# Kernel tuning notes

Hardware: AMD Instinct MI355X
Metric: run time of the kernel (lower is better)

Reference implementation:

```python
import jax, jax.numpy as jnp
import numpy as np
from jax import lax

DN = ('NCHW', 'OIHW', 'NCHW')


def conv_s2(x, w, b):
    # Conv2d(kernel=4, stride=2, padding=1): halves H,W
    y = lax.conv_general_dilated(x, w, (2, 2), ((1, 1), (1, 1)), dimension_numbers=DN)
    return y + b[None, :, None, None]


def conv_1x1(x, w, b):
    y = lax.conv_general_dilated(x, w, (1, 1), ((0, 0), (0, 0)), dimension_numbers=DN)
    return y + b[None, :, None, None]


def convT_s2(x, w, b):
    # torch ConvTranspose2d(kernel=4, stride=2, padding=1); torch weight layout [I,O,kh,kw]
    wt = jnp.flip(w, (2, 3)).transpose(1, 0, 2, 3)  # -> [O,I,kh,kw], spatially flipped
    y = lax.conv_general_dilated(x, wt, (1, 1), ((2, 2), (2, 2)),
                                 lhs_dilation=(2, 2), dimension_numbers=DN)
    return y + b[None, :, None, None]


def setup_inputs() -> dict:
    key = jax.random.key(0)
    ks = jax.random.split(key, 20)
    f32 = jnp.float32
    s = 0.05  # small init scale to keep activations sane
    inp = {
        'x': jax.random.uniform(ks[0], (32, 3, 256, 256), dtype=f32),
        # encoder
        'ew1': jax.random.normal(ks[1], (128, 3, 4, 4), f32) * s,
        'eb1': jnp.zeros((128,), f32),
        'ew2': jax.random.normal(ks[2], (256, 128, 4, 4), f32) * s,
        'eb2': jnp.zeros((256,), f32),
        'ew3': jax.random.normal(ks[3], (512, 256, 4, 4), f32) * s,
        'eb3': jnp.zeros((512,), f32),
        # pre-VQ 1x1 conv
        'pw': jax.random.normal(ks[4], (64, 512, 1, 1), f32) * s,
        'pb': jnp.zeros((64,), f32),
        # codebook (torch.randn in module)
        'emb': jax.random.normal(ks[5], (512, 64), f32),
        # decoder (ConvTranspose2d weights: [in, out, kh, kw])
        'dw1': jax.random.normal(ks[6], (64, 256, 4, 4), f32) * s,
        'db1': jnp.zeros((256,), f32),
        'dw2': jax.random.normal(ks[7], (256, 128, 4, 4), f32) * s,
        'db2': jnp.zeros((128,), f32),
        'dw3': jax.random.normal(ks[8], (128, 3, 4, 4), f32) * s,
        'db3': jnp.zeros((3,), f32),
    }
    return inp


def reference(x, ew1, eb1, ew2, eb2, ew3, eb3, pw, pb, emb,
              dw1, db1, dw2, db2, dw3, db3):
    # encoder
    h = jax.nn.relu(conv_s2(x, ew1, eb1))
    h = jax.nn.relu(conv_s2(h, ew2, eb2))
    h = jax.nn.relu(conv_s2(h, ew3, eb3))
    z_e = conv_1x1(h, pw, pb)  # [B, D, H, W]

    b, d, hh, ww = z_e.shape
    x_flat = z_e.reshape(b, d, hh * ww).transpose(0, 2, 1)  # [B, HW, D]
    # squared distances via expansion (same math, no [B,HW,K,D] blowup)
    x2 = jnp.sum(x_flat ** 2, axis=-1, keepdims=True)        # [B, HW, 1]
    e2 = jnp.sum(emb ** 2, axis=-1)                          # [K]
    dist = x2 - 2.0 * jnp.einsum('bnd,kd->bnk', x_flat, emb) + e2[None, None, :]
    indices = jnp.argmin(dist, axis=2)                       # [B, HW]
    zq_flat = emb[indices]                                   # [B, HW, D]
    z_q = zq_flat.transpose(0, 2, 1).reshape(b, d, hh, ww)

    quant_loss = (jnp.mean((zq_flat - x_flat) ** 2) * 2.0)   # matches detach-symmetric mse in fwd value

    # decoder
    y = jax.nn.relu(convT_s2(z_q, dw1, db1))
    y = jax.nn.relu(convT_s2(y, dw2, db2))
    y = jax.nn.sigmoid(convT_s2(y, dw3, db3))
    return (y, quant_loss)
```

## Files before the change

### kernel.cpp

```cpp
#include <hip/hip_runtime.h>
#include <cstddef>
#include <cstdint>

typedef __attribute__((ext_vector_type(8))) _Float16 half8;
typedef __attribute__((ext_vector_type(4))) float f32x4;

static __device__ __forceinline__ unsigned packhl(float v) {
  _Float16 h = (_Float16)v;
  _Float16 l = (_Float16)((v - (float)h) * 2048.0f);
  return (unsigned)__builtin_bit_cast(unsigned short, h) |
         ((unsigned)__builtin_bit_cast(unsigned short, l) << 16);
}


template<int CIN>
__global__ __launch_bounds__(256) void wsplit_k(
    const float* __restrict__ W, _Float16* __restrict__ Wh,
    _Float16* __restrict__ Wl, int Cout) {
  constexpr int NCB = CIN / 32;
  int idx = blockIdx.x * 256 + threadIdx.x;
  if (idx >= Cout * CIN) return;
  int ci = idx % CIN, co = idx / CIN;
  int cb = ci >> 5, k8 = (ci >> 3) & 3, j = ci & 7;
  const float* wp = W + (size_t)idx * 16;
#pragma unroll
  for (int tap = 0; tap < 16; ++tap) {
    float w = wp[tap];
    _Float16 wh = (_Float16)w;
    _Float16 wl = (_Float16)((w - (float)wh) * 2048.0f);
    size_t o = (((size_t)(tap * NCB + cb) * 4 + k8) * Cout + co) * 8 + j;
    Wh[o] = wh; Wl[o] = wl;
  }
}

template<int CIN>
__global__ __launch_bounds__(256) void wsplitT_k(
    const float* __restrict__ W, _Float16* __restrict__ Wh,
    _Float16* __restrict__ Wl, int Cout) {
  constexpr int NCB = CIN / 32;
  int idx = blockIdx.x * 256 + threadIdx.x;
  if (idx >= CIN * Cout) return;
  int co = idx % Cout, ci = idx / Cout;
  int cb = ci >> 5, k8 = (ci >> 3) & 3, j = ci & 7;
  const float* wp = W + (size_t)idx * 16;
#pragma unroll
  for (int t = 0; t < 16; ++t) {
    int py = (t >> 3) & 1, px = (t >> 2) & 1, i0 = (t >> 1) & 1, i1 = t & 1;
    int kh = py ? (i0 ? 2 : 0) : (i0 ? 3 : 1);
    int kw = px ? (i1 ? 2 : 0) : (i1 ? 3 : 1);
    float w = wp[kh * 4 + kw];
    _Float16 wh = (_Float16)w;
    _Float16 wl = (_Float16)((w - (float)wh) * 2048.0f);
    size_t o = (((size_t)(t * NCB + cb) * 4 + k8) * Cout + co) * 8 + j;
    Wh[o] = wh; Wl[o] = wl;
  }
}

__global__ __launch_bounds__(256) void border_k(
    char* base, int c8n, int H2, int W2, size_t SAI, size_t LOFF, int nimg) {
  int nb = 2 * W2 + 2 * (H2 - 2);
  int tot = nimg * c8n * 2 * nb;
  int idx = blockIdx.x * 256 + threadIdx.x;
  if (idx >= tot) return;
  int s = idx % nb; int r = idx / nb;
  int pl = r & 1; r >>= 1;
  int c8 = r % c8n; int b = r / c8n;
  int y, x;
  if (s < W2)            { y = 0;       x = s; }
  else if (s < 2 * W2)   { y = H2 - 1;  x = s - W2; }
  else { int t = s - 2 * W2; y = 1 + (t >> 1); x = (t & 1) ? W2 - 1 : 0; }
  size_t PLANE = (size_t)H2 * W2 * 16;
  char* p = base + (size_t)b * SAI + (size_t)pl * LOFF + (size_t)c8 * PLANE
            + ((size_t)y * W2 + x) * 16;
  *(uint4*)p = make_uint4(0, 0, 0, 0);
}

template<int CIN, int COUT, int CGRP, int NF, int RELU, int PACKOUT, int SPLITIN,
         int XMAP>
__global__ __launch_bounds__(256) void conv_mfma2(
    const void* __restrict__ inP, const _Float16* __restrict__ Whg,
    const _Float16* __restrict__ Wlg, const float* __restrict__ bias,
    float* __restrict__ out, int Hin, int Win, size_t inSAI, size_t inLOFF) {
  constexpr int NCB  = CIN / 32;
  constexpr int MT   = COUT / CGRP;
  constexpr int MF   = MT / 64;
  constexpr int ROWS = 2 * NF + 2;
  constexpr int NPOS = ROWS * 34;
  constexpr int K8S  = NPOS + 6;
  const int Hout = Hin >> 1, Wout = Win >> 1;
  const int TW = Wout >> 4;
  __shared__ half8 Bh[4 * K8S], Bl[4 * K8S];
  const int tid = threadIdx.x;
  const int lane = tid & 63, w = tid >> 6;
  const int l15 = lane & 15, k8 = lane >> 4;
  int tx, ty, cg, b;
  {
    unsigned nwg = gridDim.x * gridDim.y;
    unsigned id  = blockIdx.y * gridDim.x + blockIdx.x;
    unsigned sw  = (id & 7) * (nwg >> 3) + (id >> 3);
    const int bx = sw % gridDim.x, by = sw / gridDim.x;
    tx = bx % TW; ty = bx / TW;
    cg = by % CGRP;
    b  = by / CGRP;
  }
  const int oy0 = ty * NF, ox0 = tx << 4;
  const int iy_org = 2 * oy0 - 1, ix_org = 2 * ox0 - 1;
  const int cbase = cg * MT + w * (MT / 4);
  const size_t HW = (size_t)Hin * Win;
  const size_t tapStride = (size_t)NCB * 4 * COUT * 8;

  unsigned goff[4];
  const char* baseh = nullptr;
  size_t PLANE = 0;
  if (SPLITIN) {
    const int W2 = Win + 2;
    PLANE = (size_t)(Hin + 2) * W2 * 16;
    constexpr int S0[4] = {0, 64, 128, NPOS - 64};
#pragma unroll
    for (int t = 0; t < 4; ++t) {
      int s = S0[t] + lane;
      int r = s / 17, c = s - r * 17;
      int hy = r >> 1, p = r & 1;
      int hx = (c << 1) | p;
      int iy = iy_org + hy + 1, ix = ix_org + hx + 1;
      goff[t] = (unsigned)(((size_t)iy * W2 + ix) * 16);
    }
    baseh = (const char*)inP + ((size_t)b * inSAI) + (size_t)w * PLANE;
  }

  f32x4 accM[MF][NF], accX[MF][NF];
#pragma unroll
  for (int m = 0; m < MF; ++m)
#pragma unroll
    for (int nf = 0; nf < NF; ++nf) {
      accM[m][nf] = f32x4{0,0,0,0};
      accX[m][nf] = f32x4{0,0,0,0};
    }

  for (int cb = 0; cb < NCB; ++cb) {
    __syncthreads();
    if (SPLITIN) {
      const char* pc = baseh + (size_t)cb * 4 * PLANE;
      char* lh = (char*)&Bh[w * K8S];
      char* ll = (char*)&Bl[w * K8S];
      constexpr int S0[4] = {0, 64, 128, NPOS - 64};
#pragma unroll
      for (int t = 0; t < 4; ++t) {
        __builtin_amdgcn_global_load_lds(
            (const __attribute__((address_space(1))) void*)(pc + goff[t]),
            (__attribute__((address_space(3))) void*)(lh + S0[t] * 16), 16, 0, 0);
        __builtin_amdgcn_global_load_lds(
            (const __attribute__((address_space(1))) void*)(pc + inLOFF + goff[t]),
            (__attribute__((address_space(3))) void*)(ll + S0[t] * 16), 16, 0, 0);
      }
    } else {
      const unsigned* inU = (const unsigned*)inP;
      for (int u = tid; u < NPOS * 4; u += 256) {
        int kk = u / NPOS, pos = u - kk * NPOS;
        int hy = pos / 34, hx = pos - hy * 34;
        int iy = iy_org + hy, ix = ix_org + hx;
        bool ok = (unsigned)iy < (unsigned)Hin && (unsigned)ix < (unsigned)Win;
        uint4 qa = {0,0,0,0}, qb = {0,0,0,0};
        if (ok) {
          const uint4* gp = (const uint4*)(inU +
              (((size_t)b * (CIN / 8) + cb * 4 + kk) * HW + (size_t)iy * Win + ix) * 8);
          qa = gp[0]; qb = gp[1];
        }
        unsigned av[8] = {qa.x, qa.y, qa.z, qa.w, qb.x, qb.y, qb.z, qb.w};
        half8 vh, vl;
#pragma unroll
        for (int j = 0; j < 8; ++j) {
          vh[j] = __builtin_bit_cast(_Float16, (unsigned short)(av[j] & 0xffffu));
          vl[j] = __builtin_bit_cast(_Float16, (unsigned short)(av[j] >> 16));
        }
        int slotBase = (hy * 2 + (hx & 1)) * 17 + (hx >> 1);
        Bh[kk * K8S + slotBase] = vh;
        Bl[kk * K8S + slotBase] = vl;
      }
    }
    __syncthreads();
    const _Float16* aph = Whg + (((size_t)cb * 4 + k8) * COUT + cbase + l15) * 8;
    const _Float16* apl = Wlg + (((size_t)cb * 4 + k8) * COUT + cbase + l15) * 8;
    half8 ah[2][MF], al[2][MF];
#pragma unroll
    for (int m = 0; m < MF; ++m) {
      ah[0][m] = *(const half8*)(aph + m * 128);
      al[0][m] = *(const half8*)(apl + m * 128);
    }
#pragma unroll
    for (int tp = 0; tp < 16; ++tp) {
      const int cur = tp & 1, nxt = cur ^ 1;
      if (tp < 15) {
#pragma unroll
        for (int m = 0; m < MF; ++m) {
          ah[nxt][m] = *(const half8*)(aph + (size_t)(tp + 1) * tapStride + m * 128);
          al[nxt][m] = *(const half8*)(apl + (size_t)(tp + 1) * tapStride + m * 128);
        }
      }
      const int kh = tp >> 2, kw = tp & 3;
      const int p = kw & 1, cidx = kw >> 1;
#pragma unroll
      for (int nf = 0; nf < NF; ++nf) {
        const int slot = k8 * K8S + ((2 * nf + kh) * 2 + p) * 17 + l15 + cidx;
        const half8 bh = Bh[slot], bl = Bl[slot];
#pragma unroll
        for (int m = 0; m < MF; ++m) {
          accM[m][nf] = __builtin_amdgcn_mfma_f32_16x16x32_f16(ah[cur][m], bh, accM[m][nf], 0, 0, 0);
          accX[m][nf] = __builtin_amdgcn_mfma_f32_16x16x32_f16(ah[cur][m], bl, accX[m][nf], 0, 0, 0);
          accX[m][nf] = __builtin_amdgcn_mfma_f32_16x16x32_f16(al[cur][m], bh, accX[m][nf], 0, 0, 0);
        }
      }
    }
  }
#pragma unroll
  for (int m = 0; m < MF; ++m)
#pragma unroll
    for (int nf = 0; nf < NF; ++nf) {
      int oy = oy0 + nf, ox = ox0 + l15;
      if (PACKOUT) {
        unsigned pk[4];
#pragma unroll
        for (int i = 0; i < 4; ++i) {
          int co = cbase + m * 16 + k8 * 4 + i;
          float v = accM[m][nf][i] + accX[m][nf][i] * (1.0f / 2048.0f) + bias[co];
          if (RELU) v = fmaxf(v, 0.0f);
          pk[i] = packhl(v);
        }
        int co8 = (cbase + m * 16 + k8 * 4) >> 3;
        int j0 = (k8 & 1) * 4;
        unsigned* outU = (unsigned*)out;
        *(uint4*)(outU + (((size_t)b * (COUT / 8) + co8) * ((size_t)Hout * Wout)
                          + (size_t)oy * Wout + ox) * 8 + j0) =
            make_uint4(pk[0], pk[1], pk[2], pk[3]);
      } else {
#pragma unroll
        for (int i = 0; i < 4; ++i) {
          int co = cbase + m * 16 + k8 * 4 + i;
          float v = accM[m][nf][i] + accX[m][nf][i] * (1.0f / 2048.0f) + bias[co];
          if (RELU) v = fmaxf(v, 0.0f);
          out[(((size_t)b * COUT + co) * Hout + oy) * Wout + ox] = v;
        }
      }
    }
}

template<int CIN, int COUT, int CGRP, int RELU, int PACKIN, int PACKOUT, int SWZ>
__global__ __launch_bounds__(256) void convT_mfma(
    const float* __restrict__ in, const _Float16* __restrict__ Whg,
    const _Float16* __restrict__ Wlg, const float* __restrict__ bias,
    float* __restrict__ out, int Hin, int Win) {
  constexpr int NCB = CIN / 32;
  constexpr int MT  = COUT / CGRP;
  constexpr int MF  = MT / 64;
  const int Hout = Hin * 2, Wout = Win * 2;
  const int TW = Win >> 4;
  __shared__ half8 Bh[4 * 72], Bl[4 * 72];
  const int tid = threadIdx.x;
  const int lane = tid & 63, w = tid >> 6;
  const int l15 = lane & 15, k8 = lane >> 4;
  int bx = blockIdx.x, by = blockIdx.y;
  if (SWZ) {
    unsigned nwg = gridDim.x * gridDim.y;
    unsigned id  = (unsigned)by * gridDim.x + bx;
    unsigned sw  = (id & 7) * (nwg >> 3) + (id >> 3);
    bx = (int)(sw % gridDim.x); by = (int)(sw / gridDim.x);
  }
  const int tx = bx % TW, ty = bx / TW;
  const int cg = by % CGRP;
  const int b  = by / CGRP;
  const int ty0 = ty << 1, tx0 = tx << 4;
  const int cbase = cg * MT + w * (MT / 4);
  const size_t HW = (size_t)Hin * Win;
  const size_t tapStride = (size_t)NCB * 4 * COUT * 8;

  f32x4 accM[MF][4][2], accX[MF][4][2];
#pragma unroll
  for (int m = 0; m < MF; ++m)
#pragma unroll
    for (int p = 0; p < 4; ++p)
#pragma unroll
      for (int nf = 0; nf < 2; ++nf) {
        accM[m][p][nf] = f32x4{0,0,0,0};
        accX[m][p][nf] = f32x4{0,0,0,0};
      }

  for (int cb = 0; cb < NCB; ++cb) {
    __syncthreads();
    for (int u = tid; u < 288; u += 256) {
      int pos = u % 72, kk = u / 72;
      int r = pos / 18, c = pos - r * 18;
      int iy = ty0 - 1 + r, ix = tx0 - 1 + c;
      bool ok = (unsigned)iy < (unsigned)Hin && (unsigned)ix < (unsigned)Win;
      half8 vh, vl;
      if (PACKIN) {
        uint4 qa = {0,0,0,0}, qb = {0,0,0,0};
        if (ok) {
          const uint4* gp = (const uint4*)((const unsigned*)in +
              (((size_t)b * (CIN / 8) + cb * 4 + kk) * HW + (size_t)iy * Win + ix) * 8);
          qa = gp[0]; qb = gp[1];
        }
        unsigned av[8] = {qa.x, qa.y, qa.z, qa.w, qb.x, qb.y, qb.z, qb.w};
#pragma unroll
        for (int j = 0; j < 8; ++j) {
          vh[j] = __builtin_bit_cast(_Float16, (unsigned short)(av[j] & 0xffffu));
          vl[j] = __builtin_bit_cast(_Float16, (unsigned short)(av[j] >> 16));
        }
      } else {
        const float* gp = in + ((size_t)b * CIN + cb * 32 + kk * 8) * HW
                          + (ptrdiff_t)iy * Win + ix;
#pragma unroll
        for (int j = 0; j < 8; ++j) {
          float x = ok ? gp[(size_t)j * HW] : 0.0f;
          _Float16 xh = (_Float16)x;
          vh[j] = xh; vl[j] = (_Float16)((x - (float)xh) * 2048.0f);
        }
      }
      Bh[kk * 72 + pos] = vh;
      Bl[kk * 72 + pos] = vl;
    }
    __syncthreads();
    const _Float16* aph = Whg + (((size_t)cb * 4 + k8) * COUT + cbase + l15) * 8;
    const _Float16* apl = Wlg + (((size_t)cb * 4 + k8) * COUT + cbase + l15) * 8;
    half8 ah[2][MF], al[2][MF];
#pragma unroll
    for (int m = 0; m < MF; ++m) {
      ah[0][m] = *(const half8*)(aph + m * 128);
      al[0][m] = *(const half8*)(apl + m * 128);
    }
#pragma unroll
    for (int t = 0; t < 16; ++t) {
      const int cur = t & 1, nxt = cur ^ 1;
      if (t < 15) {
#pragma unroll
        for (int m = 0; m < MF; ++m) {
          ah[nxt][m] = *(const half8*)(aph + (size_t)(t + 1) * tapStride + m * 128);
          al[nxt][m] = *(const half8*)(apl + (size_t)(t + 1) * tapStride + m * 128);
        }
      }
      const int py = (t >> 3) & 1, px = (t >> 2) & 1;
      const int i0 = (t >> 1) & 1, i1 = t & 1;
      const int dy = py ? (i0 ? 0 : 1) : (i0 ? -1 : 0);
      const int dx = px ? (i1 ? 0 : 1) : (i1 ? -1 : 0);
      const int p = py * 2 + px;
#pragma unroll
      for (int nf = 0; nf < 2; ++nf) {
        int slot = k8 * 72 + (nf + 1 + dy) * 18 + (l15 + 1 + dx);
        half8 bh = Bh[slot], bl = Bl[slot];
#pragma unroll
        for (int m = 0; m < MF; ++m) {
          accM[m][p][nf] = __builtin_amdgcn_mfma_f32_16x16x32_f16(ah[cur][m], bh, accM[m][p][nf], 0, 0, 0);
          accX[m][p][nf] = __builtin_amdgcn_mfma_f32_16x16x32_f16(ah[cur][m], bl, accX[m][p][nf], 0, 0, 0);
          accX[m][p][nf] = __builtin_amdgcn_mfma_f32_16x16x32_f16(al[cur][m], bh, accX[m][p][nf], 0, 0, 0);
        }
      }
    }
  }
#pragma unroll
  for (int m = 0; m < MF; ++m) {
    const int co0m = cbase + m * 16;
#pragma unroll
    for (int nf = 0; nf < 2; ++nf) {
#pragma unroll
      for (int i = 0; i < 4; ++i) {
        int co = co0m + k8 * 4 + i;
        float bb = bias[co];
#pragma unroll
        for (int py = 0; py < 2; ++py) {
          float v0 = accM[m][py * 2 + 0][nf][i] + accX[m][py * 2 + 0][nf][i] * (1.0f / 2048.0f) + bb;
          float v1 = accM[m][py * 2 + 1][nf][i] + accX[m][py * 2 + 1][nf][i] * (1.0f / 2048.0f) + bb;
          if (RELU) { v0 = fmaxf(v0, 0.0f); v1 = fmaxf(v1, 0.0f); }
          int oy = 2 * (ty0 + nf) + py, ox = 2 * (tx0 + l15);
          if (PACKOUT) {
            unsigned* outU = (unsigned*)out;
            int co8 = (co0m >> 3) + (k8 >> 1);
            int j = (k8 * 4 + i) & 7;
            size_t base = ((size_t)b * (COUT / 8) + co8) * ((size_t)Hout * Wout);
            outU[(base + (size_t)oy * Wout + ox) * 8 + j]     = packhl(v0);
            outU[(base + (size_t)oy * Wout + ox + 1) * 8 + j] = packhl(v1);
          } else {
            *(float2*)(out + (((size_t)b * COUT + co) * Hout + oy) * Wout + ox) =
                make_float2(v0, v1);
          }
        }
      }
    }
  }
}


template<int CIN, int G, int RELU, int PACKOUT>
__global__ __launch_bounds__(256) void conv_t(
    const float* __restrict__ in, const float* __restrict__ wt,
    const float* __restrict__ bias, float* __restrict__ out,
    int Cout, int Hin, int Win, size_t oSAI, size_t oLOFF) {
  const int Hout = Hin >> 1, Wout = Win >> 1;
  const int TW = Wout >> 4;
  __shared__ float tile[34 * 35];
  int tid = threadIdx.x;
  int oxl = tid & 15, oyl = tid >> 4;
  int tyt = blockIdx.x / TW, txt = blockIdx.x - tyt * TW;
  int oy0 = tyt << 4, ox0 = txt << 4;
  int cg = blockIdx.y % (Cout / G);
  int b  = blockIdx.y / (Cout / G);
  int co0 = cg * G;
  const int iy_org = 2 * oy0 - 1, ix_org = 2 * ox0 - 1;
  const float* ip = in + (size_t)b * CIN * Hin * Win;
  float acc[G];
#pragma unroll
  for (int j = 0; j < G; ++j) acc[j] = bias[co0 + j];
  const int lbase = (2 * oyl) * 35 + 2 * oxl;
  for (int ci = 0; ci < CIN; ++ci) {
    const float* ic = ip + (size_t)ci * Hin * Win;
    __syncthreads();
#pragma unroll
    for (int k = 0; k < 5; ++k) {
      int idx = tid + k * 256;
      if (idx < 34 * 34) {
        int r = idx / 34, c = idx - r * 34;
        int iy = iy_org + r, ix = ix_org + c;
        float v = ((unsigned)iy < (unsigned)Hin && (unsigned)ix < (unsigned)Win)
                      ? ic[(size_t)iy * Win + ix] : 0.0f;
        tile[r * 35 + c] = v;
      }
    }
    __syncthreads();
    float xv[16];
#pragma unroll
    for (int kh = 0; kh < 4; ++kh)
#pragma unroll
      for (int kw = 0; kw < 4; ++kw)
        xv[kh * 4 + kw] = tile[lbase + kh * 35 + kw];
    const float* wc = wt + ((size_t)co0 * CIN + ci) * 16;
#pragma unroll
    for (int j = 0; j < G; ++j) {
      const float* wj = wc + (size_t)j * CIN * 16;
#pragma unroll
      for (int t2 = 0; t2 < 16; ++t2) acc[j] = fmaf(xv[t2], wj[t2], acc[j]);
    }
  }
  int oy = oy0 + oyl, ox = ox0 + oxl;
  if (RELU) {
#pragma unroll
    for (int j = 0; j < G; ++j) acc[j] = fmaxf(acc[j], 0.0f);
  }
  if (PACKOUT == 2) {
    const int W2 = Wout + 2;
    const size_t PLANE = (size_t)(Hout + 2) * W2 * 16;
    char* ob0 = (char*)out + (size_t)b * oSAI
                + ((size_t)(oy + 1) * W2 + ox + 1) * 16;
#pragma unroll
    for (int mb = 0; mb < G / 8; ++mb) {
      half8 hv, lv;
#pragma unroll
      for (int j = 0; j < 8; ++j) {
        float v = acc[mb * 8 + j];
        _Float16 h = (_Float16)v;
        hv[j] = h; lv[j] = (_Float16)((v - (float)h) * 2048.0f);
      }
      char* ob = ob0 + (size_t)((co0 >> 3) + mb) * PLANE;
      *(half8*)ob = hv;
      *(half8*)(ob + oLOFF) = lv;
    }
  } else {
    size_t cs = (size_t)Hout * Wout;
    float* op = out + ((size_t)(b * Cout + co0) * Hout + oy) * Wout + ox;
#pragma unroll
    for (int j = 0; j < G; ++j) op[(size_t)j * cs] = acc[j];
  }
}

template<int CIN, int G>
__global__ __launch_bounds__(256) void conv1x1_k(
    const float* __restrict__ in, const float* __restrict__ wt,
    const float* __restrict__ bias, float* __restrict__ out,
    int Cout, int HW) {
  int hw = blockIdx.x * 256 + threadIdx.x;
  int cg = blockIdx.y % (Cout / G);
  int b  = blockIdx.y / (Cout / G);
  int co0 = cg * G;
  const float* ip = in + (size_t)b * CIN * HW + hw;
  float acc[G];
#pragma unroll
  for (int j = 0; j < G; ++j) acc[j] = bias[co0 + j];
#pragma unroll 4
  for (int ci = 0; ci < CIN; ++ci) {
    float xv = ip[(size_t)ci * HW];
#pragma unroll
    for (int j = 0; j < G; ++j)
      acc[j] = fmaf(xv, wt[(size_t)(co0 + j) * CIN + ci], acc[j]);
  }
  float* op = out + ((size_t)(b * Cout + co0)) * HW + hw;
#pragma unroll
  for (int j = 0; j < G; ++j) op[(size_t)j * HW] = acc[j];
}

__global__ __launch_bounds__(128) void vq_k(
    const float* __restrict__ ze, const float* __restrict__ emb,
    float* __restrict__ zq, float* __restrict__ partial) {
  __shared__ float4 se4[128 * 16];
  __shared__ float red[128];
  int tid = threadIdx.x;
  int gid = blockIdx.x * 128 + tid;
  int b = gid >> 10, n = gid & 1023;
  const float* zp = ze + ((size_t)b << 16) + n;
  float4 v4[16];
#pragma unroll
  for (int d = 0; d < 16; ++d) {
    v4[d].x = zp[(size_t)(4 * d + 0) << 10];
    v4[d].y = zp[(size_t)(4 * d + 1) << 10];
    v4[d].z = zp[(size_t)(4 * d + 2) << 10];
    v4[d].w = zp[(size_t)(4 * d + 3) << 10];
  }
  float best = 1e30f; int bi = 0;
  for (int c = 0; c < 4; ++c) {
    __syncthreads();
    for (int i = tid; i < 2048; i += 128)
      se4[i] = ((const float4*)emb)[(c << 11) + i];
    __syncthreads();
    for (int k = 0; k < 128; ++k) {
      const float4* e = se4 + (k << 4);
      float s = 0.0f;
#pragma unroll
      for (int d = 0; d < 16; ++d) {
        float4 ev = e[d];
        float t0 = v4[d].x - ev.x; s = fmaf(t0, t0, s);
        float t1 = v4[d].y - ev.y; s = fmaf(t1, t1, s);
        float t2 = v4[d].z - ev.z; s = fmaf(t2, t2, s);
        float t3 = v4[d].w - ev.w; s = fmaf(t3, t3, s);
      }
      if (s < best) { best = s; bi = (c << 7) + k; }
    }
  }
  const float4* eb4 = (const float4*)emb + ((size_t)bi << 4);
  float* qp = zq + ((size_t)b << 16) + n;
  float ls = 0.0f;
#pragma unroll
  for (int d = 0; d < 16; ++d) {
    float4 q = eb4[d];
    qp[(size_t)(4 * d + 0) << 10] = q.x;
    qp[(size_t)(4 * d + 1) << 10] = q.y;
    qp[(size_t)(4 * d + 2) << 10] = q.z;
    qp[(size_t)(4 * d + 3) << 10] = q.w;
    float t0 = q.x - v4[d].x; ls = fmaf(t0, t0, ls);
    float t1 = q.y - v4[d].y; ls = fmaf(t1, t1, ls);
    float t2 = q.z - v4[d].z; ls = fmaf(t2, t2, ls);
    float t3 = q.w - v4[d].w; ls = fmaf(t3, t3, ls);
  }
  red[tid] = ls;
  __syncthreads();
  for (int s = 64; s > 0; s >>= 1) {
    if (tid < s) red[tid] += red[tid + s];
    __syncthreads();
  }
  if (tid == 0) partial[blockIdx.x] = red[0];
}

__global__ __launch_bounds__(256) void loss_fin(
    const float* __restrict__ partial, float* __restrict__ out) {
  __shared__ float red[256];
  int t = threadIdx.x;
  red[t] = partial[t];
  __syncthreads();
  for (int s = 128; s > 0; s >>= 1) {
    if (t < s) red[t] += red[t + s];
    __syncthreads();
  }
  if (t == 0) out[0] = red[0] * (2.0f / 2097152.0f);
}

template<int CIN, int G, int ACT>
__global__ __launch_bounds__(256) void convT_t(
    const float* __restrict__ in, const float* __restrict__ wt,
    const float* __restrict__ bias, float* __restrict__ out,
    int Cout, int Hin, int Win) {
  const int Hout = Hin * 2, Wout = Win * 2;
  const int TW = Win >> 4;
  __shared__ float tile[18 * 19];
  int tid = threadIdx.x;
  int txl = tid & 15, tyl = tid >> 4;
  int tyt = blockIdx.x / TW, txt = blockIdx.x - tyt * TW;
  int ty0 = tyt << 4, tx0 = txt << 4;
  int og = blockIdx.y % (Cout / G);
  int b  = blockIdx.y / (Cout / G);
  int o0 = og * G;
  const int iy_org = ty0 - 1, ix_org = tx0 - 1;
  const float* ip = in + (size_t)b * CIN * Hin * Win;
  float a00[G], a01[G], a10[G], a11[G];
#pragma unroll
  for (int j = 0; j < G; ++j) {
    float bb = bias[o0 + j];
    a00[j] = bb; a01[j] = bb; a10[j] = bb; a11[j] = bb;
  }
  const int lb = tyl * 19 + txl;
  for (int i = 0; i < CIN; ++i) {
    const float* ic = ip + (size_t)i * Hin * Win;
    __syncthreads();
#pragma unroll
    for (int k = 0; k < 2; ++k) {
      int idx = tid + k * 256;
      if (idx < 18 * 18) {
        int r = idx / 18, c = idx - r * 18;
        int iy = iy_org + r, ix = ix_org + c;
        float v = ((unsigned)iy < (unsigned)Hin && (unsigned)ix < (unsigned)Win)
                      ? ic[(size_t)iy * Win + ix] : 0.0f;
        tile[r * 19 + c] = v;
      }
    }
    __syncthreads();
    float x00 = tile[lb],          x01 = tile[lb + 1],      x02 = tile[lb + 2];
    float x10 = tile[lb + 19],     x11 = tile[lb + 20],     x12 = tile[lb + 21];
    float x20 = tile[lb + 38],     x21 = tile[lb + 39],     x22 = tile[lb + 40];
    const float* wv = wt + ((size_t)i * Cout + o0) * 16;
#pragma unroll
    for (int j = 0; j < G; ++j) {
      const float* w4 = wv + j * 16;
      a00[j] = fmaf(x11, w4[5],  fmaf(x10, w4[7],  fmaf(x01, w4[13], fmaf(x00, w4[15], a00[j]))));
      a01[j] = fmaf(x12, w4[4],  fmaf(x11, w4[6],  fmaf(x02, w4[12], fmaf(x01, w4[14], a01[j]))));
      a10[j] = fmaf(x21, w4[1],  fmaf(x20, w4[3],  fmaf(x11, w4[9],  fmaf(x10, w4[11], a10[j]))));
      a11[j] = fmaf(x22, w4[0],  fmaf(x21, w4[2],  fmaf(x12, w4[8],  fmaf(x11, w4[10], a11[j]))));
    }
  }
  size_t cs = (size_t)Hout * Wout;
  int ty = ty0 + tyl, tx = tx0 + txl;
  size_t base = ((size_t)(b * Cout + o0) * Hout + 2 * (size_t)ty) * Wout + 2 * tx;
#pragma unroll
  for (int j = 0; j < G; ++j) {
    float v00 = a00[j], v01 = a01[j], v10 = a10[j], v11 = a11[j];
    if (ACT == 1) {
      v00 = fmaxf(v00, 0.0f); v01 = fmaxf(v01, 0.0f);
      v10 = fmaxf(v10, 0.0f); v11 = fmaxf(v11, 0.0f);
    } else if (ACT == 2) {
      v00 = 1.0f / (1.0f + expf(-v00)); v01 = 1.0f / (1.0f + expf(-v01));
      v10 = 1.0f / (1.0f + expf(-v10)); v11 = 1.0f / (1.0f + expf(-v11));
    }
    *(float2*)(out + base + (size_t)j * cs)        = make_float2(v00, v01);
    *(float2*)(out + base + (size_t)j * cs + Wout) = make_float2(v10, v11);
  }
}

extern "C" void kernel_launch(void* const* d_in, const int* in_sizes, int n_in,
                              void* d_out, int out_size, void* d_ws, size_t ws_size,
                              hipStream_t stream) {
  const float* x   = (const float*)d_in[0];
  const float* ew1 = (const float*)d_in[1];
  const float* eb1 = (const float*)d_in[2];
  const float* ew2 = (const float*)d_in[3];
  const float* eb2 = (const float*)d_in[4];
  const float* ew3 = (const float*)d_in[5];
  const float* eb3 = (const float*)d_in[6];
  const float* pw  = (const float*)d_in[7];
  const float* pb  = (const float*)d_in[8];
  const float* emb = (const float*)d_in[9];
  const float* dw1 = (const float*)d_in[10];
  const float* db1 = (const float*)d_in[11];
  const float* dw2 = (const float*)d_in[12];
  const float* db2 = (const float*)d_in[13];
  const float* dw3 = (const float*)d_in[14];
  const float* db3 = (const float*)d_in[15];
  float* out = (float*)d_out;
  char* ws = (char*)d_ws;

  const size_t H1PLANE = 130ull * 130ull * 16ull;
  const size_t H1LOFF  = 16ull * H1PLANE;
  const size_t SAI     = 2ull * H1LOFF;
  const size_t PER  = SAI + 4194304ull + 2ull * 262144ull;
  const size_t WEXT = 4096ull + 13631488ull;
  int CB = 32;
  while (CB > 1 && (size_t)CB * PER + WEXT > ws_size) CB >>= 1;
  const size_t SA = (size_t)CB * SAI;
  const size_t SB = (size_t)CB * 4194304ull;
  const size_t SC = (size_t)CB * 262144ull;
  float* A    = (float*)(ws);
  float* Bp   = (float*)(ws + SA);
  float* ze   = (float*)(ws + SA + SB);
  float* zq   = (float*)(ws + SA + SB + SC);
  float* part = (float*)(ws + SA + SB + 2 * SC);
  _Float16* wh2  = (_Float16*)(ws + SA + SB + 2 * SC + 4096);
  _Float16* wl2  = wh2 + 524288;
  _Float16* wh3  = wl2 + 524288;
  _Float16* wl3  = wh3 + 2097152;
  _Float16* whT1 = wl3 + 2097152;
  _Float16* wlT1 = whT1 + 262144;
  _Float16* whT2 = wlT1 + 262144;
  _Float16* wlT2 = whT2 + 524288;

  wsplit_k<128><<<128, 256, 0, stream>>>(ew2, wh2, wl2, 256);
  wsplit_k<256><<<512, 256, 0, stream>>>(ew3, wh3, wl3, 512);
  wsplitT_k<64><<<64,  256, 0, stream>>>(dw1, whT1, wlT1, 256);
  wsplitT_k<256><<<128, 256, 0, stream>>>(dw2, whT2, wlT2, 128);

  for (int c0 = 0; c0 < 32; c0 += CB) {
    const float* xc = x + (size_t)c0 * 3 * 65536;
    float* outc = out + (size_t)c0 * 3 * 65536;
    {
      int nb = 2 * 130 + 2 * 128;
      int tot = CB * 16 * 2 * nb;
      border_k<<<(tot + 255) / 256, 256, 0, stream>>>(
          (char*)A, 16, 130, 130, SAI, H1LOFF, CB);
    }
    conv_t<3, 16, 1, 2><<<dim3(64, CB * 8), 256, 0, stream>>>(
        xc, ew1, eb1, A, 128, 256, 256, SAI, H1LOFF);
    conv_mfma2<128, 256, 1, 2, 1, 1, 1, 0><<<dim3(128, CB), 256, 0, stream>>>(
        (const void*)A, wh2, wl2, eb2, Bp, 128, 128, SAI, H1LOFF);
    conv_mfma2<256, 512, 2, 2, 1, 0, 0, 0><<<dim3(32, CB * 2), 256, 0, stream>>>(
        (const void*)Bp, wh3, wl3, eb3, A, 64, 64, 0, 0);
    conv1x1_k<512, 4><<<dim3(4, CB * 16), 256, 0, stream>>>(A, pw, pb, ze, 64, 1024);
    vq_k<<<CB * 8, 128, 0, stream>>>(ze, emb, zq, part + (size_t)c0 * 8);
    convT_mfma<64, 256, 4, 1, 0, 1, 1><<<dim3(32, CB * 4), 256, 0, stream>>>(
        zq, whT1, wlT1, db1, Bp, 32, 32);
    convT_mfma<256, 128, 1, 1, 1, 0, 1><<<dim3(128, CB), 256, 0, stream>>>(
        Bp, whT2, wlT2, db2, A, 64, 64);
    convT_t<128, 3, 2><<<dim3(64, CB * 1), 256, 0, stream>>>(A, dw3, db3, outc, 3, 128, 128);
  }
  loss_fin<<<1, 256, 0, stream>>>(part, out + (size_t)(out_size - 1));
}
```

Baseline: 2.514 ms.

## Double-buffer LDS staging in conv_mfma2 and split convT2 output channels

```diff
diff --git a/kernel.cpp b/kernel.cpp
--- a/kernel.cpp
+++ b/kernel.cpp
@@ -75,8 +75,7 @@
   *(uint4*)p = make_uint4(0, 0, 0, 0);
 }
 
-template<int CIN, int COUT, int CGRP, int NF, int RELU, int PACKOUT, int SPLITIN,
-         int XMAP>
+template<int CIN, int COUT, int CGRP, int NF, int RELU, int PACKOUT, int SPLITIN>
 __global__ __launch_bounds__(256) void conv_mfma2(
     const void* __restrict__ inP, const _Float16* __restrict__ Whg,
     const _Float16* __restrict__ Wlg, const float* __restrict__ bias,
@@ -87,9 +86,12 @@
   constexpr int ROWS = 2 * NF + 2;
   constexpr int NPOS = ROWS * 34;
   constexpr int K8S  = NPOS + 6;
+  constexpr int NTOT = NPOS * 4;
+  constexpr int NK   = (NTOT + 255) / 256;
   const int Hout = Hin >> 1, Wout = Win >> 1;
   const int TW = Wout >> 4;
-  __shared__ half8 Bh[4 * K8S], Bl[4 * K8S];
+  __shared__ half8 Bh0[4 * K8S], Bl0[4 * K8S];
+  __shared__ half8 Bh1[SPLITIN ? 4 * K8S : 1], Bl1[SPLITIN ? 4 * K8S : 1];
   const int tid = threadIdx.x;
   const int lane = tid & 63, w = tid >> 6;
   const int l15 = lane & 15, k8 = lane >> 4;
@@ -127,6 +129,72 @@
     }
     baseh = (const char*)inP + ((size_t)b * inSAI) + (size_t)w * PLANE;
   }
+  auto dmaStage = [&](half8* BH, half8* BL, int cb) {
+    const char* pc = baseh + (size_t)cb * 4 * PLANE;
+    char* lh = (char*)(BH + (size_t)w * K8S);
+    char* ll = (char*)(BL + (size_t)w * K8S);
+    constexpr int S0[4] = {0, 64, 128, NPOS - 64};
+#pragma unroll
+    for (int t = 0; t < 4; ++t) {
+      __builtin_amdgcn_global_load_lds(
+          (const __attribute__((address_space(1))) void*)(pc + goff[t]),
+          (__attribute__((address_space(3))) void*)(lh + S0[t] * 16), 16, 0, 0);
+      __builtin_amdgcn_global_load_lds(
+          (const __attribute__((address_space(1))) void*)(pc + inLOFF + goff[t]),
+          (__attribute__((address_space(3))) void*)(ll + S0[t] * 16), 16, 0, 0);
+    }
+  };
+
+  unsigned pBase[NK]; unsigned short pSlot[NK]; unsigned char pKk[NK];
+  bool pOk[NK], pSt[NK];
+  uint4 pfa[NK], pfb[NK];
+  if (!SPLITIN) {
+#pragma unroll
+    for (int k = 0; k < NK; ++k) {
+      int u = tid + k * 256;
+      bool st = u < NTOT;
+      int uu = st ? u : 0;
+      int kk = uu / NPOS, pos = uu - kk * NPOS;
+      int hy = pos / 34, hx = pos - hy * 34;
+      int iy = iy_org + hy, ix = ix_org + hx;
+      bool ok = st && (unsigned)iy < (unsigned)Hin && (unsigned)ix < (unsigned)Win;
+      pSt[k] = st; pOk[k] = ok;
+      pKk[k] = (unsigned char)kk;
+      pSlot[k] = (unsigned short)((hy * 2 + (hx & 1)) * 17 + (hx >> 1));
+      pBase[k] = (unsigned)((((size_t)b * (CIN / 8) + kk) * HW
+                            + (size_t)iy * Win + ix) * 2);
+    }
+  }
+  auto loadPF = [&](int cb) {
+    const uint4* inU4 = (const uint4*)inP;
+    unsigned coff = (unsigned)(cb * 4) * (unsigned)(HW * 2);
+#pragma unroll
+    for (int k = 0; k < NK; ++k) {
+      uint4 z = make_uint4(0, 0, 0, 0);
+      pfa[k] = z; pfb[k] = z;
+      if (pOk[k]) {
+        const uint4* gp = inU4 + (size_t)pBase[k] + coff;
+        pfa[k] = gp[0]; pfb[k] = gp[1];
+      }
+    }
+  };
+  auto storePF = [&](half8* BH, half8* BL) {
+#pragma unroll
+    for (int k = 0; k < NK; ++k) {
+      if (pSt[k]) {
+        unsigned av[8] = {pfa[k].x, pfa[k].y, pfa[k].z, pfa[k].w,
+                          pfb[k].x, pfb[k].y, pfb[k].z, pfb[k].w};
+        half8 vh, vl;
+#pragma unroll
+        for (int j = 0; j < 8; ++j) {
+          vh[j] = __builtin_bit_cast(_Float16, (unsigned short)(av[j] & 0xffffu));
+          vl[j] = __builtin_bit_cast(_Float16, (unsigned short)(av[j] >> 16));
+        }
+        BH[(int)pKk[k] * K8S + (int)pSlot[k]] = vh;
+        BL[(int)pKk[k] * K8S + (int)pSlot[k]] = vl;
+      }
+    }
+  };
 
   f32x4 accM[MF][NF], accX[MF][NF];
 #pragma unroll
@@ -137,48 +205,7 @@
       accX[m][nf] = f32x4{0,0,0,0};
     }
 
-  for (int cb = 0; cb < NCB; ++cb) {
-    __syncthreads();
-    if (SPLITIN) {
-      const char* pc = baseh + (size_t)cb * 4 * PLANE;
-      char* lh = (char*)&Bh[w * K8S];
-      char* ll = (char*)&Bl[w * K8S];
-      constexpr int S0[4] = {0, 64, 128, NPOS - 64};
-#pragma unroll
-      for (int t = 0; t < 4; ++t) {
-        __builtin_amdgcn_global_load_lds(
-            (const __attribute__((address_space(1))) void*)(pc + goff[t]),
-            (__attribute__((address_space(3))) void*)(lh + S0[t] * 16), 16, 0, 0);
-        __builtin_amdgcn_global_load_lds(
-            (const __attribute__((address_space(1))) void*)(pc + inLOFF + goff[t]),
-            (__attribute__((address_space(3))) void*)(ll + S0[t] * 16), 16, 0, 0);
-      }
-    } else {
-      const unsigned* inU = (const unsigned*)inP;
-      for (int u = tid; u < NPOS * 4; u += 256) {
-        int kk = u / NPOS, pos = u - kk * NPOS;
-        int hy = pos / 34, hx = pos - hy * 34;
-        int iy = iy_org + hy, ix = ix_org + hx;
-        bool ok = (unsigned)iy < (unsigned)Hin && (unsigned)ix < (unsigned)Win;
-        uint4 qa = {0,0,0,0}, qb = {0,0,0,0};
-        if (ok) {
-          const uint4* gp = (const uint4*)(inU +
-              (((size_t)b * (CIN / 8) + cb * 4 + kk) * HW + (size_t)iy * Win + ix) * 8);
-          qa = gp[0]; qb = gp[1];
-        }
-        unsigned av[8] = {qa.x, qa.y, qa.z, qa.w, qb.x, qb.y, qb.z, qb.w};
-        half8 vh, vl;
-#pragma unroll
-        for (int j = 0; j < 8; ++j) {
-          vh[j] = __builtin_bit_cast(_Float16, (unsigned short)(av[j] & 0xffffu));
-          vl[j] = __builtin_bit_cast(_Float16, (unsigned short)(av[j] >> 16));
-        }
-        int slotBase = (hy * 2 + (hx & 1)) * 17 + (hx >> 1);
-        Bh[kk * K8S + slotBase] = vh;
-        Bl[kk * K8S + slotBase] = vl;
-      }
-    }
-    __syncthreads();
+  auto computeCB = [&](const half8* BH, const half8* BL, int cb) {
     const _Float16* aph = Whg + (((size_t)cb * 4 + k8) * COUT + cbase + l15) * 8;
     const _Float16* apl = Wlg + (((size_t)cb * 4 + k8) * COUT + cbase + l15) * 8;
     half8 ah[2][MF], al[2][MF];
@@ -202,7 +229,7 @@
 #pragma unroll
       for (int nf = 0; nf < NF; ++nf) {
         const int slot = k8 * K8S + ((2 * nf + kh) * 2 + p) * 17 + l15 + cidx;
-        const half8 bh = Bh[slot], bl = Bl[slot];
+        const half8 bh = BH[slot], bl = BL[slot];
 #pragma unroll
         for (int m = 0; m < MF; ++m) {
           accM[m][nf] = __builtin_amdgcn_mfma_f32_16x16x32_f16(ah[cur][m], bh, accM[m][nf], 0, 0, 0);
@@ -211,7 +238,31 @@
         }
       }
     }
-  }
+  };
+
+  if (SPLITIN) {
+    dmaStage(Bh0, Bl0, 0);
+    for (int cb = 0; cb < NCB; cb += 2) {
+      __syncthreads();
+      if (cb + 1 < NCB) dmaStage(Bh1, Bl1, cb + 1);
+      computeCB(Bh0, Bl0, cb);
+      if (cb + 1 < NCB) {
+        __syncthreads();
+        if (cb + 2 < NCB) dmaStage(Bh0, Bl0, cb + 2);
+        computeCB(Bh1, Bl1, cb + 1);
+      }
+    }
+  } else {
+    loadPF(0);
+    for (int cb = 0; cb < NCB; ++cb) {
+      __syncthreads();
+      storePF(Bh0, Bl0);
+      __syncthreads();
+      if (cb + 1 < NCB) loadPF(cb + 1);
+      computeCB(Bh0, Bl0, cb);
+    }
+  }
+
 #pragma unroll
   for (int m = 0; m < MF; ++m)
 #pragma unroll
@@ -700,15 +751,15 @@
     }
     conv_t<3, 16, 1, 2><<<dim3(64, CB * 8), 256, 0, stream>>>(
         xc, ew1, eb1, A, 128, 256, 256, SAI, H1LOFF);
-    conv_mfma2<128, 256, 1, 2, 1, 1, 1, 0><<<dim3(128, CB), 256, 0, stream>>>(
+    conv_mfma2<128, 256, 1, 2, 1, 1, 1><<<dim3(128, CB), 256, 0, stream>>>(
         (const void*)A, wh2, wl2, eb2, Bp, 128, 128, SAI, H1LOFF);
-    conv_mfma2<256, 512, 2, 2, 1, 0, 0, 0><<<dim3(32, CB * 2), 256, 0, stream>>>(
+    conv_mfma2<256, 512, 2, 2, 1, 0, 0><<<dim3(32, CB * 2), 256, 0, stream>>>(
         (const void*)Bp, wh3, wl3, eb3, A, 64, 64, 0, 0);
     conv1x1_k<512, 4><<<dim3(4, CB * 16), 256, 0, stream>>>(A, pw, pb, ze, 64, 1024);
     vq_k<<<CB * 8, 128, 0, stream>>>(ze, emb, zq, part + (size_t)c0 * 8);
     convT_mfma<64, 256, 4, 1, 0, 1, 1><<<dim3(32, CB * 4), 256, 0, stream>>>(
         zq, whT1, wlT1, db1, Bp, 32, 32);
-    convT_mfma<256, 128, 1, 1, 1, 0, 1><<<dim3(128, CB), 256, 0, stream>>>(
+    convT_mfma<256, 128, 2, 1, 1, 0, 1><<<dim3(128, CB * 2), 256, 0, stream>>>(
         Bp, whT2, wlT2, db2, A, 64, 64);
     convT_t<128, 3, 2><<<dim3(64, CB * 1), 256, 0, stream>>>(A, dw3, db3, outc, 3, 128, 128);
   }
```

Result: slower. 2.615 ms (+4.0%).

## Emit layer-2 output as padded split hi/lo planes and split convT2 channels

Applied to the files above, without the earlier changes.

```diff
diff --git a/kernel.cpp b/kernel.cpp
--- a/kernel.cpp
+++ b/kernel.cpp
@@ -3,6 +3,7 @@
 #include <cstdint>
 
 typedef __attribute__((ext_vector_type(8))) _Float16 half8;
+typedef __attribute__((ext_vector_type(4))) _Float16 half4;
 typedef __attribute__((ext_vector_type(4))) float f32x4;
 
 static __device__ __forceinline__ unsigned packhl(float v) {
@@ -75,12 +76,12 @@
   *(uint4*)p = make_uint4(0, 0, 0, 0);
 }
 
-template<int CIN, int COUT, int CGRP, int NF, int RELU, int PACKOUT, int SPLITIN,
-         int XMAP>
+template<int CIN, int COUT, int CGRP, int NF, int RELU, int PACKOUT, int SPLITIN>
 __global__ __launch_bounds__(256) void conv_mfma2(
     const void* __restrict__ inP, const _Float16* __restrict__ Whg,
     const _Float16* __restrict__ Wlg, const float* __restrict__ bias,
-    float* __restrict__ out, int Hin, int Win, size_t inSAI, size_t inLOFF) {
+    float* __restrict__ out, int Hin, int Win,
+    size_t inSAI, size_t inLOFF, size_t outSAI, size_t outLOFF) {
   constexpr int NCB  = CIN / 32;
   constexpr int MT   = COUT / CGRP;
   constexpr int MF   = MT / 64;
@@ -217,7 +218,25 @@
 #pragma unroll
     for (int nf = 0; nf < NF; ++nf) {
       int oy = oy0 + nf, ox = ox0 + l15;
-      if (PACKOUT) {
+      if (PACKOUT == 2) {
+        const int W2o = Wout + 2;
+        const size_t PLANEo = (size_t)(Hout + 2) * W2o * 16;
+        half4 hv, lv;
+#pragma unroll
+        for (int i = 0; i < 4; ++i) {
+          int co = cbase + m * 16 + k8 * 4 + i;
+          float v = accM[m][nf][i] + accX[m][nf][i] * (1.0f / 2048.0f) + bias[co];
+          if (RELU) v = fmaxf(v, 0.0f);
+          _Float16 h = (_Float16)v;
+          hv[i] = h; lv[i] = (_Float16)((v - (float)h) * 2048.0f);
+        }
+        int c8 = (cbase + m * 16 + k8 * 4) >> 3;
+        int j0 = (k8 & 1) * 4;
+        char* ob = (char*)out + (size_t)b * outSAI + (size_t)c8 * PLANEo
+                   + (((size_t)(oy + 1) * W2o) + ox + 1) * 16 + j0 * 2;
+        *(half4*)ob = hv;
+        *(half4*)(ob + outLOFF) = lv;
+      } else if (PACKOUT == 1) {
         unsigned pk[4];
 #pragma unroll
         for (int i = 0; i < 4; ++i) {
@@ -663,12 +682,15 @@
   const size_t H1PLANE = 130ull * 130ull * 16ull;
   const size_t H1LOFF  = 16ull * H1PLANE;
   const size_t SAI     = 2ull * H1LOFF;
-  const size_t PER  = SAI + 4194304ull + 2ull * 262144ull;
+  const size_t H2PLANE = 66ull * 66ull * 16ull;
+  const size_t H2LOFF  = 32ull * H2PLANE;
+  const size_t SBI     = 2ull * H2LOFF;
+  const size_t PER  = SAI + SBI + 2ull * 262144ull;
   const size_t WEXT = 4096ull + 13631488ull;
   int CB = 32;
   while (CB > 1 && (size_t)CB * PER + WEXT > ws_size) CB >>= 1;
   const size_t SA = (size_t)CB * SAI;
-  const size_t SB = (size_t)CB * 4194304ull;
+  const size_t SB = (size_t)CB * SBI;
   const size_t SC = (size_t)CB * 262144ull;
   float* A    = (float*)(ws);
   float* Bp   = (float*)(ws + SA);
@@ -693,22 +715,26 @@
     const float* xc = x + (size_t)c0 * 3 * 65536;
     float* outc = out + (size_t)c0 * 3 * 65536;
     {
-      int nb = 2 * 130 + 2 * 128;
-      int tot = CB * 16 * 2 * nb;
-      border_k<<<(tot + 255) / 256, 256, 0, stream>>>(
+      int nb1 = 2 * 130 + 2 * 128;
+      int tot1 = CB * 16 * 2 * nb1;
+      border_k<<<(tot1 + 255) / 256, 256, 0, stream>>>(
           (char*)A, 16, 130, 130, SAI, H1LOFF, CB);
+      int nb2 = 2 * 66 + 2 * 64;
+      int tot2 = CB * 32 * 2 * nb2;
+      border_k<<<(tot2 + 255) / 256, 256, 0, stream>>>(
+          (char*)Bp, 32, 66, 66, SBI, H2LOFF, CB);
     }
     conv_t<3, 16, 1, 2><<<dim3(64, CB * 8), 256, 0, stream>>>(
         xc, ew1, eb1, A, 128, 256, 256, SAI, H1LOFF);
-    conv_mfma2<128, 256, 1, 2, 1, 1, 1, 0><<<dim3(128, CB), 256, 0, stream>>>(
-        (const void*)A, wh2, wl2, eb2, Bp, 128, 128, SAI, H1LOFF);
-    conv_mfma2<256, 512, 2, 2, 1, 0, 0, 0><<<dim3(32, CB * 2), 256, 0, stream>>>(
-        (const void*)Bp, wh3, wl3, eb3, A, 64, 64, 0, 0);
+    conv_mfma2<128, 256, 1, 2, 1, 2, 1><<<dim3(128, CB), 256, 0, stream>>>(
+        (const void*)A, wh2, wl2, eb2, Bp, 128, 128, SAI, H1LOFF, SBI, H2LOFF);
+    conv_mfma2<256, 512, 2, 2, 1, 0, 1><<<dim3(32, CB * 2), 256, 0, stream>>>(
+        (const void*)Bp, wh3, wl3, eb3, A, 64, 64, SBI, H2LOFF, 0, 0);
     conv1x1_k<512, 4><<<dim3(4, CB * 16), 256, 0, stream>>>(A, pw, pb, ze, 64, 1024);
     vq_k<<<CB * 8, 128, 0, stream>>>(ze, emb, zq, part + (size_t)c0 * 8);
     convT_mfma<64, 256, 4, 1, 0, 1, 1><<<dim3(32, CB * 4), 256, 0, stream>>>(
         zq, whT1, wlT1, db1, Bp, 32, 32);
-    convT_mfma<256, 128, 1, 1, 1, 0, 1><<<dim3(128, CB), 256, 0, stream>>>(
+    convT_mfma<256, 128, 2, 1, 1, 0, 1><<<dim3(128, CB * 2), 256, 0, stream>>>(
         Bp, whT2, wlT2, db2, A, 64, 64);
     convT_t<128, 3, 2><<<dim3(64, CB * 1), 256, 0, stream>>>(A, dw3, db3, outc, 3, 128, 128);
   }
```

After: 2.431 ms. -3.3%, faster.
